# Optimization experiments

Measured on AMD Instinct MI355X. Metric: run time of the kernel, lower is better.

## Reference

```python
import jax, jax.numpy as jnp
import numpy as np


def blend_act(x):
    # x>0: 0.9*x + 0.1*tanh(x); else 0.5*tanh(x)
    t = jnp.tanh(x)
    return jnp.where(x > 0, x * 0.9 + t * 0.1, t * 0.5)


def setup_inputs() -> dict:
    key = jax.random.key(0)
    ks = jax.random.split(key, 7)
    B, D_in, H, C = 32768, 512, 1024, 10
    x = jax.random.normal(ks[0], (B, D_in), dtype=jnp.float32)
    s1 = 1.0 / np.sqrt(D_in)
    s2 = 1.0 / np.sqrt(H)
    s3 = 1.0 / np.sqrt(H // 2)
    W1 = jax.random.uniform(ks[1], (D_in, H), jnp.float32, -s1, s1)
    b1 = jax.random.uniform(ks[2], (H,), jnp.float32, -s1, s1)
    W2 = jax.random.uniform(ks[3], (H, H // 2), jnp.float32, -s2, s2)
    b2 = jax.random.uniform(ks[4], (H // 2,), jnp.float32, -s2, s2)
    W3 = jax.random.uniform(ks[5], (H // 2, C), jnp.float32, -s3, s3)
    b3 = jax.random.uniform(ks[6], (C,), jnp.float32, -s3, s3)
    return {"x": x, "W1": W1, "b1": b1, "W2": W2, "b2": b2, "W3": W3, "b3": b3}


def reference(x, W1, b1, W2, b2, W3, b3):
    h = blend_act(x @ W1 + b1)
    # dropout is identity in eval/inference mode
    h = jax.nn.relu(h @ W2 + b2)
    return h @ W3 + b3
```

## Files before the change

### kernel.cpp

```cpp
#include <hip/hip_runtime.h>
#include <hip/hip_bf16.h>
#include <hip/hip_fp16.h>
#include <cstdint>

typedef __attribute__((ext_vector_type(8))) short s16x8;
typedef __attribute__((ext_vector_type(8))) _Float16 f16x8;
typedef __attribute__((ext_vector_type(4))) float f32x4;

__device__ __forceinline__ void gload16(const void* g, void* l){
  __builtin_amdgcn_global_load_lds((const __attribute__((address_space(1))) void*)g,
                                   (__attribute__((address_space(3))) void*)l, 16, 0, 0);
}

__global__ void transpose_f16(const float* __restrict__ in, ushort* __restrict__ outT,
                              int K, int N){
  __shared__ float tile[32][33];
  const int kb = blockIdx.y * 32, nb = blockIdx.x * 32;
  const int tx = threadIdx.x & 31, ty = threadIdx.x >> 5;
#pragma unroll
  for (int r = 0; r < 32; r += 8)
    tile[ty + r][tx] = in[(size_t)(kb + ty + r) * N + nb + tx];
  __syncthreads();
#pragma unroll
  for (int r = 0; r < 32; r += 8){
    const float v = tile[tx][ty + r];
    const _Float16 h = (_Float16)v;
    outT[(size_t)(nb + ty + r) * K + kb + tx] = __builtin_bit_cast(ushort, h);
  }
}

__global__ void finish_out(const float* __restrict__ part, const float* __restrict__ b3,
                           float* __restrict__ out){
  const int idx = blockIdx.x * 256 + threadIdx.x;
  if (idx >= 32768 * 10) return;
  out[idx] = b3[idx % 10] + part[idx] + part[327680 + idx];
}

template<int MODE>
__global__ __launch_bounds__(256, 2)
void gemm_f16_128x256(const void* __restrict__ Asrc, const ushort* __restrict__ Bw,
                      const float* __restrict__ bias, ushort* __restrict__ outH,
                      const float* __restrict__ W3, float* __restrict__ part,
                      int N, int K)
{
  __shared__ ushort lds[MODE == 0 ? 32768 : 36992];
  const int t = threadIdx.x;
  const int lane = t & 63;
  const int wn = t >> 6;
  const int ln15 = lane & 15, lnHi = lane >> 4;

  const int gx = gridDim.x;
  const int nwg = gx * gridDim.y;
  const int bid = blockIdx.y * gx + blockIdx.x;
  const int swz = (bid & 7) * (nwg >> 3) + (bid >> 3);
  const int m0 = (swz / gx) * 128;
  const int n0 = (swz % gx) * 256;

  const ushort* gB = Bw + (size_t)n0 * K;

  if constexpr (MODE == 1){
    ushort* w3lds = &lds[32768];
#pragma unroll
    for (int i2 = 0; i2 < 16; ++i2){
      const int idx = i2 * 256 + t;
      const int c = idx >> 8, k = idx & 255;
      const float v = (c < 10) ? W3[(size_t)(n0 + k) * 10 + c] : 0.f;
      w3lds[c * 264 + k] = __builtin_bit_cast(ushort, (_Float16)v);
    }
  }

  const int rh0  = t >> 3;
  const int slot = t & 7;
  const int gkhw = ((slot << 4) ^ ((rh0 & 7) << 4)) >> 1;
  const uint dA = (uint)(rh0 * 64 + slot * 8);
  const uint dB = (uint)(8192 + rh0 * 64 + slot * 8);
  const ushort* pB = gB + (size_t)rh0 * K + gkhw;
  const float*  pAf = (const float*)Asrc + ((size_t)(m0 + rh0)) * K + slot * 8;
  const uint    dAw = (uint)(rh0 * 64 + ((slot ^ (rh0 & 7)) << 3));
  const ushort* pAh = (const ushort*)Asrc + ((size_t)(m0 + rh0)) * K + gkhw;

  const int swb = (ln15 & 7) << 4;
  const int koff0 = ((lnHi * 16) ^ swb) >> 1;
  const int koff1 = koff0 ^ 32;
  const int hA = ln15 * 64;
  const int hB = 8192 + (wn * 64 + ln15) * 64;

  f32x4 acc[8][4] = {};

  auto loadA = [&](f32x4 (&av)[4][2], int kt){
#pragma unroll
    for (int c = 0; c < 4; ++c){
      const float* src = pAf + (size_t)c * 32 * K + kt;
      av[c][0] = *(const f32x4*)src;
      av[c][1] = *(const f32x4*)(src + 4);
    }
  };
  auto writeA = [&](const f32x4 (&av)[4][2]){
#pragma unroll
    for (int c = 0; c < 4; ++c){
      f16x8 hv;
#pragma unroll
      for (int j = 0; j < 4; ++j){
        hv[j]     = (_Float16)av[c][0][j];
        hv[4 + j] = (_Float16)av[c][1][j];
      }
      *(f16x8*)&lds[dAw + c * 2048] = hv;
    }
  };
  auto stageB = [&](int kt){
#pragma unroll
    for (int c = 0; c < 8; ++c)
      gload16(pB + (size_t)c * 32 * K + kt, &lds[dB + c * 2048]);
  };
  auto mfmaTile = [&](){
    {
      f16x8 af[8], bfv[4];
#pragma unroll
      for (int m = 0; m < 8; ++m)
        af[m] = *(const f16x8*)&lds[hA + m * 1024 + koff0];
#pragma unroll
      for (int j = 0; j < 4; ++j)
        bfv[j] = *(const f16x8*)&lds[hB + j * 1024 + koff0];
      __builtin_amdgcn_s_setprio(1);
#pragma unroll
      for (int m = 0; m < 8; ++m)
#pragma unroll
        for (int j = 0; j < 4; ++j)
          acc[m][j] = __builtin_amdgcn_mfma_f32_16x16x32_f16(af[m], bfv[j], acc[m][j], 0, 0, 0);
      __builtin_amdgcn_s_setprio(0);
    }
    __builtin_amdgcn_sched_barrier(0);
    {
      f16x8 af[8], bfv[4];
#pragma unroll
      for (int m = 0; m < 8; ++m)
        af[m] = *(const f16x8*)&lds[hA + m * 1024 + koff1];
#pragma unroll
      for (int j = 0; j < 4; ++j)
        bfv[j] = *(const f16x8*)&lds[hB + j * 1024 + koff1];
      __builtin_amdgcn_s_setprio(1);
#pragma unroll
      for (int m = 0; m < 8; ++m)
#pragma unroll
        for (int j = 0; j < 4; ++j)
          acc[m][j] = __builtin_amdgcn_mfma_f32_16x16x32_f16(af[m], bfv[j], acc[m][j], 0, 0, 0);
      __builtin_amdgcn_s_setprio(0);
    }
  };

  if constexpr (MODE == 0){
    f32x4 avA[4][2], avB[4][2];
    loadA(avA, 0);
    for (int kt = 0; kt < K; kt += 128){
      __syncthreads();
      stageB(kt);
      writeA(avA);
      loadA(avB, kt + 64);
      __syncthreads();
      mfmaTile();
      __syncthreads();
      stageB(kt + 64);
      writeA(avB);
      loadA(avA, (kt + 128 < K) ? kt + 128 : 0);
      __syncthreads();
      mfmaTile();
    }
  } else {
    for (int kt = 0; kt < K; kt += 64){
      __syncthreads();
#pragma unroll
      for (int c = 0; c < 4; ++c)
        gload16(pAh + (size_t)c * 32 * K + kt, &lds[dA + c * 2048]);
      stageB(kt);
      __syncthreads();
      mfmaTile();
    }
  }

  __syncthreads();

  const int rowbase = lnHi * 4;
  const int colbase = wn * 64 + ln15;
#pragma unroll
  for (int j = 0; j < 4; ++j){
    const int col = colbase + j * 16;
    const float bv = bias[n0 + col];
#pragma unroll
    for (int i = 0; i < 8; ++i){
#pragma unroll
      for (int r = 0; r < 4; ++r){
        const int row = rowbase + i * 16 + r;
        const float v = acc[i][j][r] + bv;
        float a;
        if (MODE == 0){
          const float th = 1.f - 2.f / (__expf(2.f * v) + 1.f);
          a = v > 0.f ? v * 0.9f + th * 0.1f : th * 0.5f;
        } else {
          a = v > 0.f ? v : 0.f;
        }
        const _Float16 h = (_Float16)a;
        lds[row * 256 + (col ^ ((row & 7) << 3))] = __builtin_bit_cast(ushort, h);
      }
    }
  }
  __syncthreads();

  if constexpr (MODE == 0){
#pragma unroll
    for (int it = 0; it < 16; ++it){
      const int chunk = it * 256 + t;
      const int row = chunk >> 5, g = chunk & 31;
      const s16x8 vv = *(const s16x8*)&lds[row * 256 + ((g ^ (row & 7)) << 3)];
      *(s16x8*)&outH[(size_t)(m0 + row) * N + n0 + (g << 3)] = vv;
    }
  } else {
    const ushort* w3lds = &lds[32768];
    const int nb = n0 >> 8;
    f32x4 p3[2] = {};
#pragma unroll
    for (int ks = 0; ks < 8; ++ks){
      const f16x8 bw = *(const f16x8*)&w3lds[ln15 * 264 + ks * 32 + lnHi * 8];
#pragma unroll
      for (int f = 0; f < 2; ++f){
        const int mr = wn * 32 + f * 16 + ln15;
        const int colhw = ks * 32 + lnHi * 8;
        const f16x8 aw = *(const f16x8*)&lds[mr * 256 + (colhw ^ ((mr & 7) << 3))];
        p3[f] = __builtin_amdgcn_mfma_f32_16x16x32_f16(aw, bw, p3[f], 0, 0, 0);
      }
    }
    const int c = ln15;
    if (c < 10){
#pragma unroll
      for (int f = 0; f < 2; ++f)
#pragma unroll
        for (int r = 0; r < 4; ++r){
          const int m = m0 + wn * 32 + f * 16 + lnHi * 4 + r;
          part[((size_t)nb * 32768 + m) * 10 + c] = p3[f][r];
        }
    }
  }
}

extern "C" void kernel_launch(void* const* d_in, const int* in_sizes, int n_in,
                              void* d_out, int out_size, void* d_ws, size_t ws_size,
                              hipStream_t stream){
  const float* x  = (const float*)d_in[0];
  const float* W1 = (const float*)d_in[1];
  const float* b1 = (const float*)d_in[2];
  const float* W2 = (const float*)d_in[3];
  const float* b2 = (const float*)d_in[4];
  const float* W3 = (const float*)d_in[5];
  const float* b3 = (const float*)d_in[6];
  float* out = (float*)d_out;

  const int B = 32768, Din = 512, H = 1024, Hh = 512;
  char* ws = (char*)d_ws;
  const size_t MB = (size_t)1 << 20;
  ushort* h1   = (ushort*)(ws);
  float*  part = (float*)(ws + 64 * MB);
  ushort* W1T  = (ushort*)(ws + 96 * MB);
  ushort* W2T  = (ushort*)(ws + 97 * MB);

  transpose_f16<<<dim3(H / 32, Din / 32), 256, 0, stream>>>(W1, W1T, Din, H);
  transpose_f16<<<dim3(Hh / 32, H / 32), 256, 0, stream>>>(W2, W2T, H, Hh);

  gemm_f16_128x256<0><<<dim3(H / 256, B / 128), 256, 0, stream>>>(
      x,  W1T, b1, h1, nullptr, nullptr, H, Din);
  gemm_f16_128x256<1><<<dim3(Hh / 256, B / 128), 256, 0, stream>>>(
      h1, W2T, b2, nullptr, W3, part, Hh, H);
  finish_out<<<(B * 10 + 255) / 256, 256, 0, stream>>>(part, b3, out);
}
```

Baseline: 112.3 us.

## Double-buffer B tiles in LDS and use partial vmcnt waits to overlap loads

Adds a second LDS buffer for the weight (B) tile, so the next k-slice's direct-to-LDS loads are issued before the current slice's MFMAs run. Full __syncthreads are replaced by raw s_barrier with explicit s_waitcnt counts, so only the older loads must finish. The W3 staging for mode 1 moves after the main loop so it can reuse the LDS, which now has a fixed size of 80KB. This aims to hide global load latency behind compute, at the cost of more LDS per block and a possible drop in occupancy.

```diff
diff --git a/kernel.cpp b/kernel.cpp
--- a/kernel.cpp
+++ b/kernel.cpp
@@ -43,7 +43,7 @@
                       const float* __restrict__ W3, float* __restrict__ part,
                       int N, int K)
 {
-  __shared__ ushort lds[MODE == 0 ? 32768 : 36992];
+  __shared__ ushort lds[40960];
   const int t = threadIdx.x;
   const int lane = t & 63;
   const int wn = t >> 6;
@@ -58,6 +58,133 @@
 
   const ushort* gB = Bw + (size_t)n0 * K;
 
+  const int rh0  = t >> 3;
+  const int slot = t & 7;
+  const int gkhw = ((slot << 4) ^ ((rh0 & 7) << 4)) >> 1;
+  const uint dA  = (uint)(rh0 * 64 + slot * 8);
+  const uint dB0 = (uint)(8192 + rh0 * 64 + slot * 8);
+  const ushort* pB = gB + (size_t)rh0 * K + gkhw;
+  const float*  pAf = (const float*)Asrc + ((size_t)(m0 + rh0)) * K + slot * 8;
+  const uint    dAw = (uint)(rh0 * 64 + ((slot ^ (rh0 & 7)) << 3));
+  const ushort* pAh = (const ushort*)Asrc + ((size_t)(m0 + rh0)) * K + gkhw;
+
+  const int swb = (ln15 & 7) << 4;
+  const int koff0 = ((lnHi * 16) ^ swb) >> 1;
+  const int koff1 = koff0 ^ 32;
+  const int hA  = ln15 * 64;
+  const int rB_ = (wn * 64 + ln15) * 64;
+
+  f32x4 acc[8][4] = {};
+
+  auto loadA = [&](f32x4 (&av)[4][2], int kt){
+#pragma unroll
+    for (int c = 0; c < 4; ++c){
+      const float* src = pAf + (size_t)c * 32 * K + kt;
+      av[c][0] = *(const f32x4*)src;
+      av[c][1] = *(const f32x4*)(src + 4);
+    }
+  };
+  auto writeA = [&](const f32x4 (&av)[4][2]){
+#pragma unroll
+    for (int c = 0; c < 4; ++c){
+      f16x8 hv;
+#pragma unroll
+      for (int j = 0; j < 4; ++j){
+        hv[j]     = (_Float16)av[c][0][j];
+        hv[4 + j] = (_Float16)av[c][1][j];
+      }
+      *(f16x8*)&lds[dAw + c * 2048] = hv;
+    }
+  };
+  auto stageB = [&](int kt, int p){
+    const uint d = dB0 + (uint)p * 16384;
+#pragma unroll
+    for (int c = 0; c < 8; ++c)
+      gload16(pB + (size_t)c * 32 * K + kt, &lds[d + c * 2048]);
+  };
+  auto mfmaTile = [&](int par){
+    const int hB = 8192 + par * 16384 + rB_;
+    {
+      f16x8 af[8], bfv[4];
+#pragma unroll
+      for (int m = 0; m < 8; ++m)
+        af[m] = *(const f16x8*)&lds[hA + m * 1024 + koff0];
+#pragma unroll
+      for (int j = 0; j < 4; ++j)
+        bfv[j] = *(const f16x8*)&lds[hB + j * 1024 + koff0];
+      __builtin_amdgcn_s_setprio(1);
+#pragma unroll
+      for (int m = 0; m < 8; ++m)
+#pragma unroll
+        for (int j = 0; j < 4; ++j)
+          acc[m][j] = __builtin_amdgcn_mfma_f32_16x16x32_f16(af[m], bfv[j], acc[m][j], 0, 0, 0);
+      __builtin_amdgcn_s_setprio(0);
+    }
+    __builtin_amdgcn_sched_barrier(0);
+    {
+      f16x8 af[8], bfv[4];
+#pragma unroll
+      for (int m = 0; m < 8; ++m)
+        af[m] = *(const f16x8*)&lds[hA + m * 1024 + koff1];
+#pragma unroll
+      for (int j = 0; j < 4; ++j)
+        bfv[j] = *(const f16x8*)&lds[hB + j * 1024 + koff1];
+      __builtin_amdgcn_s_setprio(1);
+#pragma unroll
+      for (int m = 0; m < 8; ++m)
+#pragma unroll
+        for (int j = 0; j < 4; ++j)
+          acc[m][j] = __builtin_amdgcn_mfma_f32_16x16x32_f16(af[m], bfv[j], acc[m][j], 0, 0, 0);
+      __builtin_amdgcn_s_setprio(0);
+    }
+  };
+
+  if constexpr (MODE == 0){
+    f32x4 avA[4][2], avB[4][2];
+    stageB(0, 0);
+    loadA(avA, 0);
+    for (int kt = 0; kt < K; kt += 128){
+      __builtin_amdgcn_s_barrier();
+      writeA(avA);
+      stageB(kt + 64, 1);
+      loadA(avB, kt + 64);
+      asm volatile("s_waitcnt lgkmcnt(0) vmcnt(16)" ::: "memory");
+      __builtin_amdgcn_s_barrier();
+      mfmaTile(0);
+      __builtin_amdgcn_s_barrier();
+      writeA(avB);
+      if (kt + 128 < K){
+        stageB(kt + 128, 0);
+        loadA(avA, kt + 128);
+        asm volatile("s_waitcnt lgkmcnt(0) vmcnt(16)" ::: "memory");
+      } else {
+        asm volatile("s_waitcnt lgkmcnt(0) vmcnt(0)" ::: "memory");
+      }
+      __builtin_amdgcn_s_barrier();
+      mfmaTile(1);
+    }
+  } else {
+    const int NT = K >> 6;
+    stageB(0, 0);
+    for (int u = 0; u < NT; ++u){
+      const int par = u & 1;
+      __builtin_amdgcn_s_barrier();
+#pragma unroll
+      for (int c = 0; c < 4; ++c)
+        gload16(pAh + (size_t)c * 32 * K + u * 64, &lds[dA + c * 2048]);
+      if (u + 1 < NT){
+        stageB((u + 1) * 64, par ^ 1);
+        asm volatile("s_waitcnt vmcnt(8)" ::: "memory");
+      } else {
+        asm volatile("s_waitcnt vmcnt(0)" ::: "memory");
+      }
+      __builtin_amdgcn_s_barrier();
+      mfmaTile(par);
+    }
+  }
+
+  __syncthreads();
+
   if constexpr (MODE == 1){
     ushort* w3lds = &lds[32768];
 #pragma unroll
@@ -68,117 +195,6 @@
       w3lds[c * 264 + k] = __builtin_bit_cast(ushort, (_Float16)v);
     }
   }
-
-  const int rh0  = t >> 3;
-  const int slot = t & 7;
-  const int gkhw = ((slot << 4) ^ ((rh0 & 7) << 4)) >> 1;
-  const uint dA = (uint)(rh0 * 64 + slot * 8);
-  const uint dB = (uint)(8192 + rh0 * 64 + slot * 8);
-  const ushort* pB = gB + (size_t)rh0 * K + gkhw;
-  const float*  pAf = (const float*)Asrc + ((size_t)(m0 + rh0)) * K + slot * 8;
-  const uint    dAw = (uint)(rh0 * 64 + ((slot ^ (rh0 & 7)) << 3));
-  const ushort* pAh = (const ushort*)Asrc + ((size_t)(m0 + rh0)) * K + gkhw;
-
-  const int swb = (ln15 & 7) << 4;
-  const int koff0 = ((lnHi * 16) ^ swb) >> 1;
-  const int koff1 = koff0 ^ 32;
-  const int hA = ln15 * 64;
-  const int hB = 8192 + (wn * 64 + ln15) * 64;
-
-  f32x4 acc[8][4] = {};
-
-  auto loadA = [&](f32x4 (&av)[4][2], int kt){
-#pragma unroll
-    for (int c = 0; c < 4; ++c){
-      const float* src = pAf + (size_t)c * 32 * K + kt;
-      av[c][0] = *(const f32x4*)src;
-      av[c][1] = *(const f32x4*)(src + 4);
-    }
-  };
-  auto writeA = [&](const f32x4 (&av)[4][2]){
-#pragma unroll
-    for (int c = 0; c < 4; ++c){
-      f16x8 hv;
-#pragma unroll
-      for (int j = 0; j < 4; ++j){
-        hv[j]     = (_Float16)av[c][0][j];
-        hv[4 + j] = (_Float16)av[c][1][j];
-      }
-      *(f16x8*)&lds[dAw + c * 2048] = hv;
-    }
-  };
-  auto stageB = [&](int kt){
-#pragma unroll
-    for (int c = 0; c < 8; ++c)
-      gload16(pB + (size_t)c * 32 * K + kt, &lds[dB + c * 2048]);
-  };
-  auto mfmaTile = [&](){
-    {
-      f16x8 af[8], bfv[4];
-#pragma unroll
-      for (int m = 0; m < 8; ++m)
-        af[m] = *(const f16x8*)&lds[hA + m * 1024 + koff0];
-#pragma unroll
-      for (int j = 0; j < 4; ++j)
-        bfv[j] = *(const f16x8*)&lds[hB + j * 1024 + koff0];
-      __builtin_amdgcn_s_setprio(1);
-#pragma unroll
-      for (int m = 0; m < 8; ++m)
-#pragma unroll
-        for (int j = 0; j < 4; ++j)
-          acc[m][j] = __builtin_amdgcn_mfma_f32_16x16x32_f16(af[m], bfv[j], acc[m][j], 0, 0, 0);
-      __builtin_amdgcn_s_setprio(0);
-    }
-    __builtin_amdgcn_sched_barrier(0);
-    {
-      f16x8 af[8], bfv[4];
-#pragma unroll
-      for (int m = 0; m < 8; ++m)
-        af[m] = *(const f16x8*)&lds[hA + m * 1024 + koff1];
-#pragma unroll
-      for (int j = 0; j < 4; ++j)
-        bfv[j] = *(const f16x8*)&lds[hB + j * 1024 + koff1];
-      __builtin_amdgcn_s_setprio(1);
-#pragma unroll
-      for (int m = 0; m < 8; ++m)
-#pragma unroll
-        for (int j = 0; j < 4; ++j)
-          acc[m][j] = __builtin_amdgcn_mfma_f32_16x16x32_f16(af[m], bfv[j], acc[m][j], 0, 0, 0);
-      __builtin_amdgcn_s_setprio(0);
-    }
-  };
-
-  if constexpr (MODE == 0){
-    f32x4 avA[4][2], avB[4][2];
-    loadA(avA, 0);
-    for (int kt = 0; kt < K; kt += 128){
-      __syncthreads();
-      stageB(kt);
-      writeA(avA);
-      loadA(avB, kt + 64);
-      __syncthreads();
-      mfmaTile();
-      __syncthreads();
-      stageB(kt + 64);
-      writeA(avB);
-      loadA(avA, (kt + 128 < K) ? kt + 128 : 0);
-      __syncthreads();
-      mfmaTile();
-    }
-  } else {
-    for (int kt = 0; kt < K; kt += 64){
-      __syncthreads();
-#pragma unroll
-      for (int c = 0; c < 4; ++c)
-        gload16(pAh + (size_t)c * 32 * K + kt, &lds[dA + c * 2048]);
-      stageB(kt);
-      __syncthreads();
-      mfmaTile();
-    }
-  }
-
-  __syncthreads();
-
   const int rowbase = lnHi * 4;
   const int colbase = wn * 64 + ln15;
 #pragma unroll
```

Result: slower. 209.5 us (+86.6%).
